# Kernel tuning notes

Hardware: AMD Instinct MI355X
Metric: run time of the kernel (lower is better)

Reference implementation:

```python
import jax, jax.numpy as jnp
import numpy as np

IN_C, HID, LSTM_H, OUT_C = 128, 128, 128, 2
N_NODES, N_EDGES, N_GRAPHS = 100000, 1600000, 256


def gcn_conv(x, src, dst, W, b, n_nodes):
    # h = XW, then symmetric-normalized aggregation with self loops (PyG GCNConv defaults)
    h = x @ W  # [N, H]
    loop = jnp.arange(n_nodes)
    s = jnp.concatenate([src, loop])
    d = jnp.concatenate([dst, loop])
    deg = jax.ops.segment_sum(jnp.ones_like(d, dtype=h.dtype), d, num_segments=n_nodes)
    dinv = jnp.where(deg > 0, jax.lax.rsqrt(deg), 0.0)
    norm = dinv[s] * dinv[d]  # [E+N]
    out = jax.ops.segment_sum(norm[:, None] * h[s], d, num_segments=n_nodes)
    return out + b


def setup_inputs() -> dict:
    key = jax.random.key(0)
    ks = jax.random.split(key, 16)
    x = jax.random.normal(ks[0], (N_NODES, IN_C), dtype=jnp.float32)
    edge_index = jax.random.randint(ks[1], (2, N_EDGES), 0, N_NODES)
    batch = jnp.sort(jax.random.randint(ks[2], (N_NODES,), 0, N_GRAPHS))
    sc = lambda *shape: 1.0 / np.sqrt(shape[0])
    W0 = jax.random.normal(ks[3], (IN_C, HID), jnp.float32) * sc(IN_C)
    b0 = jnp.zeros((HID,), jnp.float32)
    W1 = jax.random.normal(ks[4], (HID, HID), jnp.float32) * sc(HID)
    b1 = jnp.zeros((HID,), jnp.float32)
    W2 = jax.random.normal(ks[5], (HID, HID), jnp.float32) * sc(HID)
    b2 = jnp.zeros((HID,), jnp.float32)
    W_ih = jax.random.normal(ks[6], (4 * LSTM_H, HID), jnp.float32) * sc(HID)
    W_hh = jax.random.normal(ks[7], (4 * LSTM_H, LSTM_H), jnp.float32) * sc(LSTM_H)
    b_ih = jnp.zeros((4 * LSTM_H,), jnp.float32)
    b_hh = jnp.zeros((4 * LSTM_H,), jnp.float32)
    W_fc = jax.random.normal(ks[8], (OUT_C, LSTM_H), jnp.float32) * sc(LSTM_H)
    b_fc = jnp.zeros((OUT_C,), jnp.float32)
    return dict(x=x, edge_index=edge_index, batch=batch, num_graphs=N_GRAPHS,
                W0=W0, b0=b0, W1=W1, b1=b1, W2=W2, b2=b2,
                W_ih=W_ih, W_hh=W_hh, b_ih=b_ih, b_hh=b_hh, W_fc=W_fc, b_fc=b_fc)


def reference(x, edge_index, batch, num_graphs, W0, b0, W1, b1, W2, b2,
              W_ih, W_hh, b_ih, b_hh, W_fc, b_fc):
    n_nodes = x.shape[0]
    src, dst = edge_index[0], edge_index[1]
    h = x
    for W, b in ((W0, b0), (W1, b1), (W2, b2)):
        h = jax.nn.relu(gcn_conv(h, src, dst, W, b, n_nodes))
    # dropout: identity in eval mode
    # global_mean_pool over batch ids
    sums = jax.ops.segment_sum(h, batch, num_segments=num_graphs)  # [G, HID]
    cnts = jax.ops.segment_sum(jnp.ones((n_nodes,), h.dtype), batch, num_segments=num_graphs)
    pooled = sums / jnp.maximum(cnts, 1.0)[:, None]
    # single-step LSTM from zero state: h0 = c0 = 0 => W_hh contributes 0
    g = pooled @ W_ih.T + b_ih + b_hh  # [G, 4H]
    i, f, gg, o = jnp.split(g, 4, axis=-1)  # PyTorch gate order i,f,g,o
    c = jax.nn.sigmoid(i) * jnp.tanh(gg)
    hn = jax.nn.sigmoid(o) * jnp.tanh(c)
    return hn @ W_fc.T + b_fc
```

## Files before the change

kernel.cpp:

```cpp
#include <hip/hip_runtime.h>
#include <math.h>
#include <stdint.h>

#define HID 128
#define SCAN_CHUNK 1024
#define NBUCK_MAX 512
#define EDGE_TILE 8192
#define GEMM_ROWS 128
#define XS_STRIDE 136

typedef short bf16x8 __attribute__((ext_vector_type(8)));
typedef float f32x4 __attribute__((ext_vector_type(4)));

__device__ __forceinline__ unsigned int f2bf(float f) {
    union { float f; uint32_t i; } u; u.f = f;
    uint32_t r = u.i + 0x7fffu + ((u.i >> 16) & 1u);
    return r >> 16;
}

__global__ __launch_bounds__(256) void scan_phase1(const int* __restrict__ cnt,
                                                   int* __restrict__ blockSums,
                                                   float* __restrict__ dinv, int nN) {
    __shared__ int sdata[256];
    const int t = threadIdx.x;
    const int idx = blockIdx.x * SCAN_CHUNK + t * 4;
    int v0 = 0, v1 = 0, v2 = 0, v3 = 0;
    if (idx + 3 < nN) {
        int4 v = *(const int4*)(cnt + idx);
        v0 = v.x; v1 = v.y; v2 = v.z; v3 = v.w;
        float4 dv;
        dv.x = rsqrtf((float)v0 + 1.0f);
        dv.y = rsqrtf((float)v1 + 1.0f);
        dv.z = rsqrtf((float)v2 + 1.0f);
        dv.w = rsqrtf((float)v3 + 1.0f);
        *(float4*)(dinv + idx) = dv;
    } else {
        if (idx     < nN) { v0 = cnt[idx];     dinv[idx]     = rsqrtf((float)v0 + 1.0f); }
        if (idx + 1 < nN) { v1 = cnt[idx + 1]; dinv[idx + 1] = rsqrtf((float)v1 + 1.0f); }
        if (idx + 2 < nN) { v2 = cnt[idx + 2]; dinv[idx + 2] = rsqrtf((float)v2 + 1.0f); }
        if (idx + 3 < nN) { v3 = cnt[idx + 3]; dinv[idx + 3] = rsqrtf((float)v3 + 1.0f); }
    }
    sdata[t] = v0 + v1 + v2 + v3;
    __syncthreads();
#pragma unroll
    for (int off = 128; off > 0; off >>= 1) {
        if (t < off) sdata[t] += sdata[t + off];
        __syncthreads();
    }
    if (t == 0) blockSums[blockIdx.x] = sdata[0];
}

__global__ __launch_bounds__(256) void scan_phase2(int* __restrict__ blockSums, int nB) {
    __shared__ int sd[256];
    const int t = threadIdx.x;
    sd[t] = (t < nB) ? blockSums[t] : 0;
    __syncthreads();
#pragma unroll
    for (int off = 1; off < 256; off <<= 1) {
        int v = sd[t];
        int add = (t >= off) ? sd[t - off] : 0;
        __syncthreads();
        sd[t] = v + add;
        __syncthreads();
    }
    if (t < nB) blockSums[t] = (t > 0) ? sd[t - 1] : 0;
}

__global__ __launch_bounds__(256) void scan_phase3(const int* __restrict__ cnt,
                                                   const int* __restrict__ blockOffsets,
                                                   int* __restrict__ rowptr, int nN, int nE) {
    __shared__ int sdata[256];
    const int t = threadIdx.x;
    const int idx = blockIdx.x * SCAN_CHUNK + t * 4;
    int v0 = 0, v1 = 0, v2 = 0, v3 = 0;
    if (idx + 3 < nN) {
        int4 v = *(const int4*)(cnt + idx);
        v0 = v.x; v1 = v.y; v2 = v.z; v3 = v.w;
    } else {
        if (idx     < nN) v0 = cnt[idx];
        if (idx + 1 < nN) v1 = cnt[idx + 1];
        if (idx + 2 < nN) v2 = cnt[idx + 2];
        if (idx + 3 < nN) v3 = cnt[idx + 3];
    }
    sdata[t] = v0 + v1 + v2 + v3;
    __syncthreads();
#pragma unroll
    for (int off = 1; off < 256; off <<= 1) {
        int v = sdata[t];
        int add = (t >= off) ? sdata[t - off] : 0;
        __syncthreads();
        sdata[t] = v + add;
        __syncthreads();
    }
    const int pre = blockOffsets[blockIdx.x] + ((t > 0) ? sdata[t - 1] : 0);
    if (idx + 3 < nN) {
        *(int4*)(rowptr + idx) = make_int4(pre, pre + v0, pre + v0 + v1, pre + v0 + v1 + v2);
    } else {
        if (idx     < nN) rowptr[idx]     = pre;
        if (idx + 1 < nN) rowptr[idx + 1] = pre + v0;
        if (idx + 2 < nN) rowptr[idx + 2] = pre + v0 + v1;
// ... 110 lines not shown
        int w = i >> 14, r = i & 16383;
        int n = r >> 7, k = r & 127;
        const float* W = (w == 0) ? W0 : (w == 1) ? W1 : W2;
        Wtb[i] = (unsigned short)f2bf(W[k * HID + n]);
    }
}

__global__ __launch_bounds__(256) void gemm_mfma_f32in(const float* __restrict__ X,
                                                       const uint4* __restrict__ Wtb,
                                                       const float* __restrict__ dinv,
                                                       unsigned int* __restrict__ Pb32,
                                                       int nN) {
    __shared__ short Xs[GEMM_ROWS * XS_STRIDE];
    __shared__ short Ws[HID * XS_STRIDE];
    const int tid = threadIdx.x;
    const int rowBase = blockIdx.x * GEMM_ROWS;
#pragma unroll
    for (int it = 0; it < 16; ++it) {
        int f = it * 256 + tid;
        int row = f >> 5, c = f & 31;
        int grow = rowBase + row;
        float4 v = make_float4(0.f, 0.f, 0.f, 0.f);
        if (grow < nN) v = *(const float4*)(X + (size_t)grow * HID + c * 4);
        uint2 o;
        o.x = f2bf(v.x) | (f2bf(v.y) << 16);
        o.y = f2bf(v.z) | (f2bf(v.w) << 16);
        *(uint2*)(&Xs[row * XS_STRIDE + c * 4]) = o;
    }
#pragma unroll
    for (int it = 0; it < 8; ++it) {
        int f = it * 256 + tid;
        int n = f >> 4, c = f & 15;
        *(uint4*)(&Ws[n * XS_STRIDE + c * 8]) = Wtb[f];
    }
    __syncthreads();
    const int wave = tid >> 6, lane = tid & 63;
    const int quad = lane >> 4, l16 = lane & 15;
    f32x4 acc[2][8] = {};
    const int kq = quad * 8;
#pragma unroll
    for (int ks = 0; ks < 4; ++ks) {
        const int k0 = ks * 32 + kq;
        bf16x8 a0 = *(const bf16x8*)(&Xs[(wave * 32 + l16) * XS_STRIDE + k0]);
        bf16x8 a1 = *(const bf16x8*)(&Xs[(wave * 32 + 16 + l16) * XS_STRIDE + k0]);
#pragma unroll
        for (int nt = 0; nt < 8; ++nt) {
            bf16x8 b = *(const bf16x8*)(&Ws[(nt * 16 + l16) * XS_STRIDE + k0]);
            acc[0][nt] = __builtin_amdgcn_mfma_f32_16x16x32_bf16(a0, b, acc[0][nt], 0, 0, 0);
            acc[1][nt] = __builtin_amdgcn_mfma_f32_16x16x32_bf16(a1, b, acc[1][nt], 0, 0, 0);
        }
    }
#pragma unroll
    for (int mt = 0; mt < 2; ++mt) {
        const int gr0 = rowBase + wave * 32 + mt * 16 + quad * 4;
#pragma unroll
        for (int r = 0; r < 4; ++r) {
            const int gr = gr0 + r;
            const bool ok = gr < nN;
            const float d = ok ? dinv[gr] : 0.f;
#pragma unroll
            for (int nt = 0; nt < 8; ++nt) {
                float v = d * acc[mt][nt][r];
                float vo = __shfl_xor(v, 1, 64);
                if (ok && !(l16 & 1)) {
                    Pb32[(size_t)gr * 64 + nt * 8 + (l16 >> 1)] = f2bf(v) | (f2bf(vo) << 16);
                }
            }
        }
    }
}

__device__ __forceinline__ void acc_bf8(const uint4 q, float* a) {
    union { uint32_t i; float f; } t;
    t.i = q.x << 16;          a[0] += t.f;
    t.i = q.x & 0xffff0000u;  a[1] += t.f;
    t.i = q.y << 16;          a[2] += t.f;
    t.i = q.y & 0xffff0000u;  a[3] += t.f;
    t.i = q.z << 16;          a[4] += t.f;
    t.i = q.z & 0xffff0000u;  a[5] += t.f;
    t.i = q.w << 16;          a[6] += t.f;
    t.i = q.w & 0xffff0000u;  a[7] += t.f;
}

__global__ __launch_bounds__(256) void fused_agg_gemm(const uint4* __restrict__ Pb,
                                                      const int* __restrict__ rowptr,
                                                      const int* __restrict__ ssrc,
                                                      const float* __restrict__ dinv,
                                                      const float* __restrict__ bias,
                                                      const uint4* __restrict__ Wtb,
                                                      unsigned int* __restrict__ Pout32,
                                                      int nN) {
    __shared__ short Ws[HID * XS_STRIDE];
    __shared__ short Hs[16 * XS_STRIDE];
    const int tid = threadIdx.x;
#pragma unroll
    for (int it = 0; it < 8; ++it) {
        int f = it * 256 + tid;
        int n = f >> 4, c = f & 15;
        *(uint4*)(&Ws[n * XS_STRIDE + c * 8]) = Wtb[f];
    }
    const int lane16 = tid & 15;
    const int grp = tid >> 4;
    const int v = blockIdx.x * 16 + grp;
    const bool ok = v < nN;
    float a0[8], a1[8], a2[8], a3[8];
#pragma unroll
    for (int i = 0; i < 8; ++i) { a0[i] = 0.f; a1[i] = 0.f; a2[i] = 0.f; a3[i] = 0.f; }
    uint4 q = make_uint4(0u, 0u, 0u, 0u);
    if (ok) {
        acc_bf8(Pb[(size_t)v * 16 + lane16], a0);
        int e = rowptr[v];
        const int e1 = rowptr[v + 1];
        for (; e + 4 <= e1; e += 4) {
            const int u0 = ssrc[e + 0], u1 = ssrc[e + 1], u2 = ssrc[e + 2], u3 = ssrc[e + 3];
            uint4 q0 = Pb[(size_t)u0 * 16 + lane16];
            uint4 q1 = Pb[(size_t)u1 * 16 + lane16];
            uint4 q2 = Pb[(size_t)u2 * 16 + lane16];
            uint4 q3 = Pb[(size_t)u3 * 16 + lane16];
            acc_bf8(q0, a0); acc_bf8(q1, a1); acc_bf8(q2, a2); acc_bf8(q3, a3);
        }
        for (; e < e1; ++e) {
            uint4 qe = Pb[(size_t)ssrc[e] * 16 + lane16];
            acc_bf8(qe, a1);
        }
        const float dv = dinv[v];
        const float4 bb0 = ((const float4*)bias)[lane16 * 2];
        const float4 bb1 = ((const float4*)bias)[lane16 * 2 + 1];
        float4 o0, o1;
        o0.x = fmaxf(fmaf(dv, (a0[0] + a1[0]) + (a2[0] + a3[0]), bb0.x), 0.f);
        o0.y = fmaxf(fmaf(dv, (a0[1] + a1[1]) + (a2[1] + a3[1]), bb0.y), 0.f);
        o0.z = fmaxf(fmaf(dv, (a0[2] + a1[2]) + (a2[2] + a3[2]), bb0.z), 0.f);
        o0.w = fmaxf(fmaf(dv, (a0[3] + a1[3]) + (a2[3] + a3[3]), bb0.w), 0.f);
        o1.x = fmaxf(fmaf(dv, (a0[4] + a1[4]) + (a2[4] + a3[4]), bb1.x), 0.f);
        o1.y = fmaxf(fmaf(dv, (a0[5] + a1[5]) + (a2[5] + a3[5]), bb1.y), 0.f);
        o1.z = fmaxf(fmaf(dv, (a0[6] + a1[6]) + (a2[6] + a3[6]), bb1.z), 0.f);
        o1.w = fmaxf(fmaf(dv, (a0[7] + a1[7]) + (a2[7] + a3[7]), bb1.w), 0.f);
        q.x = f2bf(o0.x) | (f2bf(o0.y) << 16);
        q.y = f2bf(o0.z) | (f2bf(o0.w) << 16);
        q.z = f2bf(o1.x) | (f2bf(o1.y) << 16);
        q.w = f2bf(o1.z) | (f2bf(o1.w) << 16);
    }
    *(uint4*)(&Hs[grp * XS_STRIDE + lane16 * 8]) = q;
    __syncthreads();
    const int wave = tid >> 6, lane = tid & 63;
    const int quad = lane >> 4, l16 = lane & 15;
    f32x4 acc[2] = {};
#pragma unroll
    for (int ks = 0; ks < 4; ++ks) {
        const int k0 = ks * 32 + quad * 8;
        bf16x8 a = *(const bf16x8*)(&Hs[l16 * XS_STRIDE + k0]);
#pragma unroll
        for (int nt = 0; nt < 2; ++nt) {
            bf16x8 b = *(const bf16x8*)(&Ws[((wave * 2 + nt) * 16 + l16) * XS_STRIDE + k0]);
            acc[nt] = __builtin_amdgcn_mfma_f32_16x16x32_bf16(a, b, acc[nt], 0, 0, 0);
        }
    }
#pragma unroll
    for (int r = 0; r < 4; ++r) {
        const int gr = blockIdx.x * 16 + quad * 4 + r;
        const bool okr = gr < nN;
        const float d = okr ? dinv[gr] : 0.f;
#pragma unroll
        for (int nt = 0; nt < 2; ++nt) {
            float val = d * acc[nt][r];
            float vo = __shfl_xor(val, 1, 64);
            if (okr && !(l16 & 1)) {
                Pout32[(size_t)gr * 64 + (wave * 2 + nt) * 8 + (l16 >> 1)] =
                    f2bf(val) | (f2bf(vo) << 16);
            }
        }
    }
}

__global__ __launch_bounds__(256) void agg_kernel(const uint4* __restrict__ Pb,
                                                  const int* __restrict__ rowptr,
                                                  const int* __restrict__ ssrc,
                                                  const float* __restrict__ dinv,
                                                  const float* __restrict__ bias,
                                                  uint4* __restrict__ Xb_out, int nN) {
    const int lane = threadIdx.x & 15;
    const int grp = threadIdx.x >> 4;
    const int v = blockIdx.x * 16 + grp;
    if (v >= nN) return;
    float a0[8], a1[8], a2[8], a3[8];
#pragma unroll
    for (int i = 0; i < 8; ++i) { a0[i] = 0.f; a1[i] = 0.f; a2[i] = 0.f; a3[i] = 0.f; }
    acc_bf8(Pb[(size_t)v * 16 + lane], a0);
    int e = rowptr[v];
    const int e1 = rowptr[v + 1];
    for (; e + 4 <= e1; e += 4) {
        const int u0 = ssrc[e + 0], u1 = ssrc[e + 1], u2 = ssrc[e + 2], u3 = ssrc[e + 3];
        uint4 q0 = Pb[(size_t)u0 * 16 + lane];
        uint4 q1 = Pb[(size_t)u1 * 16 + lane];
        uint4 q2 = Pb[(size_t)u2 * 16 + lane];
        uint4 q3 = Pb[(size_t)u3 * 16 + lane];
        acc_bf8(q0, a0); acc_bf8(q1, a1); acc_bf8(q2, a2); acc_bf8(q3, a3);
    }
    for (; e < e1; ++e) {
        uint4 q = Pb[(size_t)ssrc[e] * 16 + lane];
        acc_bf8(q, a1);
    }
    const float dv = dinv[v];
    const float4 bb0 = ((const float4*)bias)[lane * 2];
    const float4 bb1 = ((const float4*)bias)[lane * 2 + 1];
    float4 o0, o1;
    o0.x = fmaxf(fmaf(dv, (a0[0] + a1[0]) + (a2[0] + a3[0]), bb0.x), 0.f);
    o0.y = fmaxf(fmaf(dv, (a0[1] + a1[1]) + (a2[1] + a3[1]), bb0.y), 0.f);
    o0.z = fmaxf(fmaf(dv, (a0[2] + a1[2]) + (a2[2] + a3[2]), bb0.z), 0.f);
    o0.w = fmaxf(fmaf(dv, (a0[3] + a1[3]) + (a2[3] + a3[3]), bb0.w), 0.f);
    o1.x = fmaxf(fmaf(dv, (a0[4] + a1[4]) + (a2[4] + a3[4]), bb1.x), 0.f);
    o1.y = fmaxf(fmaf(dv, (a0[5] + a1[5]) + (a2[5] + a3[5]), bb1.y), 0.f);
    o1.z = fmaxf(fmaf(dv, (a0[6] + a1[6]) + (a2[6] + a3[6]), bb1.z), 0.f);
    o1.w = fmaxf(fmaf(dv, (a0[7] + a1[7]) + (a2[7] + a3[7]), bb1.w), 0.f);
    uint4 q;
    q.x = f2bf(o0.x) | (f2bf(o0.y) << 16);
    q.y = f2bf(o0.z) | (f2bf(o0.w) << 16);
    q.z = f2bf(o1.x) | (f2bf(o1.y) << 16);
    q.w = f2bf(o1.z) | (f2bf(o1.w) << 16);
    Xb_out[(size_t)v * 16 + lane] = q;
}

__global__ __launch_bounds__(256) void pool_partial(const unsigned int* __restrict__ Xb32,
                                                    const int* __restrict__ batch,
                                                    float* __restrict__ psum, int nN) {
    const int c2 = threadIdx.x & 63;
    int n = blockIdx.x * 64 + (threadIdx.x >> 6);
    const int nEnd = min(blockIdx.x * 64 + 64, nN);
    float acc0 = 0.f, acc1 = 0.f;
    int g = -1;
    for (; n < nEnd; n += 4) {
        int gn = batch[n];
        unsigned int q = Xb32[(size_t)n * 64 + c2];
        union { uint32_t i; float f; } lo, hi;
        lo.i = q << 16; hi.i = q & 0xffff0000u;
        if (gn != g) {
            if (g >= 0) {
                atomicAdd(&psum[g * HID + c2 * 2], acc0);
                atomicAdd(&psum[g * HID + c2 * 2 + 1], acc1);
            }
            g = gn;
            acc0 = lo.f; acc1 = hi.f;
        } else {
            acc0 += lo.f; acc1 += hi.f;
        }
    }
    if (g >= 0) {
        atomicAdd(&psum[g * HID + c2 * 2], acc0);
        atomicAdd(&psum[g * HID + c2 * 2 + 1], acc1);
    }
}

__global__ __launch_bounds__(128) void pool_finalize(const float* __restrict__ psum,
                                                     const int* __restrict__ batch,
                                                     float* __restrict__ pooled, int nN) {
    const int g = blockIdx.x;
    int lo = 0, hi = nN;
    while (lo < hi) { int m = (lo + hi) >> 1; if (batch[m] < g) lo = m + 1; else hi = m; }
    const int start = lo;
    hi = nN;
    while (lo < hi) { int m = (lo + hi) >> 1; if (batch[m] < g + 1) lo = m + 1; else hi = m; }
    const float c = (float)max(lo - start, 1);
    pooled[g * HID + threadIdx.x] = psum[g * HID + threadIdx.x] / c;
}

__device__ __forceinline__ float sigmoidf_(float x) { return 1.0f / (1.0f + expf(-x)); }

__global__ __launch_bounds__(128) void lstm_fc_kernel(const float* __restrict__ pooled,
                                                      const float* __restrict__ W_ih,
                                                      const float* __restrict__ b_ih,
                                                      const float* __restrict__ b_hh,
                                                      const float* __restrict__ W_fc,
                                                      const float* __restrict__ b_fc,
                                                      float* __restrict__ out) {
    __shared__ float pv[HID];
    __shared__ float r0[2], r1[2];
    const int g = blockIdx.x, j = threadIdx.x;
    pv[j] = pooled[g * HID + j];
    __syncthreads();
    float di = b_ih[j] + b_hh[j];
    float dg = b_ih[256 + j] + b_hh[256 + j];
    float dO = b_ih[384 + j] + b_hh[384 + j];
    const float4* pv4 = (const float4*)pv;
#pragma unroll 4
    for (int k4 = 0; k4 < 32; ++k4) {
        float4 p = pv4[k4];
        float4 wi = *(const float4*)(W_ih + (size_t)j * HID + k4 * 4);
        float4 wg = *(const float4*)(W_ih + (size_t)(256 + j) * HID + k4 * 4);
        float4 wo = *(const float4*)(W_ih + (size_t)(384 + j) * HID + k4 * 4);
        di += p.x * wi.x + p.y * wi.y + p.z * wi.z + p.w * wi.w;
        dg += p.x * wg.x + p.y * wg.y + p.z * wg.z + p.w * wg.w;
        dO += p.x * wo.x + p.y * wo.y + p.z * wo.z + p.w * wo.w;
    }
    float c = sigmoidf_(di) * tanhf(dg);
    float hn = sigmoidf_(dO) * tanhf(c);
    float p0 = hn * W_fc[j];
    float p1 = hn * W_fc[HID + j];
#pragma unroll
    for (int off = 32; off > 0; off >>= 1) {
        p0 += __shfl_down(p0, off, 64);
        p1 += __shfl_down(p1, off, 64);
    }
    const int w = j >> 6, l = j & 63;
    if (l == 0) { r0[w] = p0; r1[w] = p1; }
    __syncthreads();
    if (j == 0) {
        out[g * 2 + 0] = r0[0] + r0[1] + b_fc[0];
        out[g * 2 + 1] = r1[0] + r1[1] + b_fc[1];
    }
}

extern "C" void kernel_launch(void* const* d_in, const int* in_sizes, int n_in,
                              void* d_out, int out_size, void* d_ws, size_t ws_size,
                              hipStream_t stream) {
    const float* x      = (const float*)d_in[0];
    const int*   eidx   = (const int*)d_in[1];
    const int*   batch  = (const int*)d_in[2];
    const float* W0     = (const float*)d_in[4];
    const float* b0     = (const float*)d_in[5];
    const float* W1     = (const float*)d_in[6];
    const float* b1     = (const float*)d_in[7];
    const float* W2     = (const float*)d_in[8];
    const float* b2     = (const float*)d_in[9];
    const float* W_ih   = (const float*)d_in[10];
    const float* b_ih   = (const float*)d_in[12];
    const float* b_hh   = (const float*)d_in[13];
    const float* W_fc   = (const float*)d_in[14];
    const float* b_fc   = (const float*)d_in[15];
    float* out = (float*)d_out;

    const int nN = in_sizes[0] / HID;
    const int nE = in_sizes[1] / 2;
    const int nG = out_size / 2;
    const int* src = eidx;
    const int* dst = eidx + nE;
    const int rowsPad = (nN + GEMM_ROWS - 1) & ~(GEMM_ROWS - 1);

    size_t off = 0;
    auto alloc = [&](size_t bytes) -> void* {
        void* p = (char*)d_ws + off;
        off += (bytes + 255) & ~(size_t)255;
        return p;
    };
    uint4* Pb     = (uint4*)alloc((size_t)nN * 16 * sizeof(uint4));
    uint4* Pb2    = (uint4*)alloc((size_t)nN * 16 * sizeof(uint4));
    uint4* Xb     = (uint4*)alloc((size_t)nN * 16 * sizeof(uint4));
    float* dinv   = (float*)alloc((size_t)nN * sizeof(float));
    int*   cnt    = (int*)alloc((size_t)nN * sizeof(int));
    int*   rowptr = (int*)alloc((size_t)(nN + 1) * sizeof(int));
    int*   ssrc   = (int*)alloc((size_t)nE * sizeof(int));
    unsigned int* ebuf = (unsigned int*)alloc((size_t)nE * sizeof(unsigned int));
    float* pooled = (float*)alloc((size_t)nG * HID * sizeof(float));
    float* psum   = (float*)alloc((size_t)nG * HID * sizeof(float));
    int*   blockSums = (int*)alloc(1024 * sizeof(int));
    int*   bcnt   = (int*)alloc(NBUCK_MAX * sizeof(int));
    int*   boff   = (int*)alloc(NBUCK_MAX * sizeof(int));
    int*   bcur   = (int*)alloc(NBUCK_MAX * sizeof(int));
    unsigned short* Wtb = (unsigned short*)alloc(3 * HID * HID * sizeof(unsigned short));
    (void)ws_size;

    const int scanBlocks = (nN + SCAN_CHUNK - 1) / SCAN_CHUNK;
    const int nB = (nN + 255) >> 8;
    const int tileBlocks = (nE + EDGE_TILE - 1) / EDGE_TILE;

    hipMemsetAsync(bcnt, 0, NBUCK_MAX * sizeof(int), stream);
    bucket_count<<<tileBlocks, 256, 0, stream>>>(dst, bcnt, nE, nB);
    bucket_scan<<<1, 512, 0, stream>>>(bcnt, boff, bcur, nB);
    bucket_scatter<<<tileBlocks, 256, 0, stream>>>(src, dst, bcur, ebuf, nE, nB);

    node_count<<<nB, 256, 0, stream>>>(ebuf, boff, cnt, nE, nB, nN);
    scan_phase1<<<scanBlocks, 256, 0, stream>>>(cnt, blockSums, dinv, nN);
    scan_phase2<<<1, 256, 0, stream>>>(blockSums, scanBlocks);
    scan_phase3<<<scanBlocks, 256, 0, stream>>>(cnt, blockSums, rowptr, nN, nE);
    csr_from_buckets<<<nB, 256, 0, stream>>>(ebuf, boff, rowptr, ssrc, nE, nB);

    wt_kernel<<<(3 * HID * HID + 255) / 256, 256, 0, stream>>>(W0, W1, W2, Wtb);

    const int gemmBlocks = rowsPad / GEMM_ROWS;
    const int aggBlocks = (nN + 15) / 16;
    const uint4* Wt1 = (const uint4*)(Wtb + HID * HID);
    const uint4* Wt2 = (const uint4*)(Wtb + 2 * HID * HID);

    gemm_mfma_f32in<<<gemmBlocks, 256, 0, stream>>>(x, (const uint4*)Wtb, dinv,
                                                    (unsigned int*)Pb, nN);
    fused_agg_gemm<<<aggBlocks, 256, 0, stream>>>(Pb, rowptr, ssrc, dinv, b0, Wt1,
                                                  (unsigned int*)Pb2, nN);
    fused_agg_gemm<<<aggBlocks, 256, 0, stream>>>(Pb2, rowptr, ssrc, dinv, b1, Wt2,
                                                  (unsigned int*)Pb, nN);
    agg_kernel<<<aggBlocks, 256, 0, stream>>>(Pb, rowptr, ssrc, dinv, b2, Xb, nN);

    hipMemsetAsync(psum, 0, (size_t)nG * HID * sizeof(float), stream);
    pool_partial<<<(nN + 63) / 64, 256, 0, stream>>>((const unsigned int*)Xb, batch, psum, nN);
    pool_finalize<<<nG, 128, 0, stream>>>(psum, batch, pooled, nN);
    lstm_fc_kernel<<<nG, 128, 0, stream>>>(pooled, W_ih, b_ih, b_hh, W_fc, b_fc, out);
}
```

Baseline: 465.3 us.

## Shuffle-broadcast edge indices, gather 8 rows in flight, load W fragments from global

Each 16-lane group now loads 8 neighbour indices in one coalesced read and broadcasts them with wave shuffles. It then issues 8 independent row gathers per iteration instead of 4 scalar-index gathers, and accumulates into 2 register arrays instead of 4. The fused aggregation+GEMM kernel no longer stages the whole 128x128 weight tile in LDS. Each wave loads its own MFMA B fragments straight from global memory into registers, which sharply cuts LDS per block and should raise occupancy. The cost is redundant global weight reads per block, which rely on L2 caching, plus some extra shuffle instructions.

New measurement: 471.5 us. Within noise of the previous version (+1.3%).

```diff
diff --git a/kernel.cpp b/kernel.cpp
--- a/kernel.cpp
+++ b/kernel.cpp
@@ -292,6 +292,60 @@
     t.i = q.w & 0xffff0000u;  a[7] += t.f;
 }
 
+__device__ __forceinline__ void gather_accum(const uint4* __restrict__ Pb,
+                                             const int* __restrict__ rowptr,
+                                             const int* __restrict__ ssrc,
+                                             int v, int lane16, int gbase,
+                                             float* __restrict__ a0,
+                                             float* __restrict__ a1) {
+    acc_bf8(Pb[(size_t)v * 16 + lane16], a0);
+    int e = rowptr[v];
+    const int e1 = rowptr[v + 1];
+    const int sl = lane16 & 7;
+    for (; e + 8 <= e1; e += 8) {
+        const int s = ssrc[e + sl];
+        const int u0 = __shfl(s, gbase + 0, 64);
+        const int u1 = __shfl(s, gbase + 1, 64);
+        const int u2 = __shfl(s, gbase + 2, 64);
+        const int u3 = __shfl(s, gbase + 3, 64);
+        uint4 q0 = Pb[(size_t)u0 * 16 + lane16];
+        uint4 q1 = Pb[(size_t)u1 * 16 + lane16];
+        uint4 q2 = Pb[(size_t)u2 * 16 + lane16];
+        uint4 q3 = Pb[(size_t)u3 * 16 + lane16];
+        const int u4 = __shfl(s, gbase + 4, 64);
+        const int u5 = __shfl(s, gbase + 5, 64);
+        const int u6 = __shfl(s, gbase + 6, 64);
+        const int u7 = __shfl(s, gbase + 7, 64);
+        uint4 q4 = Pb[(size_t)u4 * 16 + lane16];
+        uint4 q5 = Pb[(size_t)u5 * 16 + lane16];
+        uint4 q6 = Pb[(size_t)u6 * 16 + lane16];
+        uint4 q7 = Pb[(size_t)u7 * 16 + lane16];
+        acc_bf8(q0, a0); acc_bf8(q1, a1); acc_bf8(q2, a0); acc_bf8(q3, a1);
+        acc_bf8(q4, a0); acc_bf8(q5, a1); acc_bf8(q6, a0); acc_bf8(q7, a1);
+    }
+    const int rem = e1 - e;
+    if (rem > 0) {
+        const int s = ssrc[(sl < rem) ? (e + sl) : e];
+        int j = 0;
+        if (rem >= 4) {
+            const int u0 = __shfl(s, gbase + 0, 64);
+            const int u1 = __shfl(s, gbase + 1, 64);
+            const int u2 = __shfl(s, gbase + 2, 64);
+            const int u3 = __shfl(s, gbase + 3, 64);
+            uint4 q0 = Pb[(size_t)u0 * 16 + lane16];
+            uint4 q1 = Pb[(size_t)u1 * 16 + lane16];
+            uint4 q2 = Pb[(size_t)u2 * 16 + lane16];
+            uint4 q3 = Pb[(size_t)u3 * 16 + lane16];
+            acc_bf8(q0, a0); acc_bf8(q1, a1); acc_bf8(q2, a0); acc_bf8(q3, a1);
+            j = 4;
+        }
+        for (; j < rem; ++j) {
+            const int u = __shfl(s, gbase + j, 64);
+            acc_bf8(Pb[(size_t)u * 16 + lane16], a1);
+        }
+    }
+}
+
 __global__ __launch_bounds__(256) void fused_agg_gemm(const uint4* __restrict__ Pb,
                                                       const int* __restrict__ rowptr,
                                                       const int* __restrict__ ssrc,
@@ -300,51 +354,31 @@
                                                       const uint4* __restrict__ Wtb,
                                                       unsigned int* __restrict__ Pout32,
                                                       int nN) {
-    __shared__ short Ws[HID * XS_STRIDE];
     __shared__ short Hs[16 * XS_STRIDE];
     const int tid = threadIdx.x;
-#pragma unroll
-    for (int it = 0; it < 8; ++it) {
-        int f = it * 256 + tid;
-        int n = f >> 4, c = f & 15;
-        *(uint4*)(&Ws[n * XS_STRIDE + c * 8]) = Wtb[f];
-    }
     const int lane16 = tid & 15;
     const int grp = tid >> 4;
+    const int gbase = tid & 48;
     const int v = blockIdx.x * 16 + grp;
     const bool ok = v < nN;
-    float a0[8], a1[8], a2[8], a3[8];
-#pragma unroll
-    for (int i = 0; i < 8; ++i) { a0[i] = 0.f; a1[i] = 0.f; a2[i] = 0.f; a3[i] = 0.f; }
+    float a0[8], a1[8];
+#pragma unroll
+    for (int i = 0; i < 8; ++i) { a0[i] = 0.f; a1[i] = 0.f; }
+    if (ok) gather_accum(Pb, rowptr, ssrc, v, lane16, gbase, a0, a1);
     uint4 q = make_uint4(0u, 0u, 0u, 0u);
     if (ok) {
-        acc_bf8(Pb[(size_t)v * 16 + lane16], a0);
-        int e = rowptr[v];
-        const int e1 = rowptr[v + 1];
-        for (; e + 4 <= e1; e += 4) {
-            const int u0 = ssrc[e + 0], u1 = ssrc[e + 1], u2 = ssrc[e + 2], u3 = ssrc[e + 3];
-            uint4 q0 = Pb[(size_t)u0 * 16 + lane16];
-            uint4 q1 = Pb[(size_t)u1 * 16 + lane16];
-            uint4 q2 = Pb[(size_t)u2 * 16 + lane16];
-            uint4 q3 = Pb[(size_t)u3 * 16 + lane16];
-            acc_bf8(q0, a0); acc_bf8(q1, a1); acc_bf8(q2, a2); acc_bf8(q3, a3);
-        }
-        for (; e < e1; ++e) {
-            uint4 qe = Pb[(size_t)ssrc[e] * 16 + lane16];
-            acc_bf8(qe, a1);
-        }
         const float dv = dinv[v];
         const float4 bb0 = ((const float4*)bias)[lane16 * 2];
         const float4 bb1 = ((const float4*)bias)[lane16 * 2 + 1];
         float4 o0, o1;
-        o0.x = fmaxf(fmaf(dv, (a0[0] + a1[0]) + (a2[0] + a3[0]), bb0.x), 0.f);
-        o0.y = fmaxf(fmaf(dv, (a0[1] + a1[1]) + (a2[1] + a3[1]), bb0.y), 0.f);
-        o0.z = fmaxf(fmaf(dv, (a0[2] + a1[2]) + (a2[2] + a3[2]), bb0.z), 0.f);
-        o0.w = fmaxf(fmaf(dv, (a0[3] + a1[3]) + (a2[3] + a3[3]), bb0.w), 0.f);
-        o1.x = fmaxf(fmaf(dv, (a0[4] + a1[4]) + (a2[4] + a3[4]), bb1.x), 0.f);
-        o1.y = fmaxf(fmaf(dv, (a0[5] + a1[5]) + (a2[5] + a3[5]), bb1.y), 0.f);
-        o1.z = fmaxf(fmaf(dv, (a0[6] + a1[6]) + (a2[6] + a3[6]), bb1.z), 0.f);
-        o1.w = fmaxf(fmaf(dv, (a0[7] + a1[7]) + (a2[7] + a3[7]), bb1.w), 0.f);
+        o0.x = fmaxf(fmaf(dv, a0[0] + a1[0], bb0.x), 0.f);
+        o0.y = fmaxf(fmaf(dv, a0[1] + a1[1], bb0.y), 0.f);
+        o0.z = fmaxf(fmaf(dv, a0[2] + a1[2], bb0.z), 0.f);
+        o0.w = fmaxf(fmaf(dv, a0[3] + a1[3], bb0.w), 0.f);
+        o1.x = fmaxf(fmaf(dv, a0[4] + a1[4], bb1.x), 0.f);
+        o1.y = fmaxf(fmaf(dv, a0[5] + a1[5], bb1.y), 0.f);
+        o1.z = fmaxf(fmaf(dv, a0[6] + a1[6], bb1.z), 0.f);
+        o1.w = fmaxf(fmaf(dv, a0[7] + a1[7], bb1.w), 0.f);
         q.x = f2bf(o0.x) | (f2bf(o0.y) << 16);
         q.y = f2bf(o0.z) | (f2bf(o0.w) << 16);
         q.z = f2bf(o1.x) | (f2bf(o1.y) << 16);
@@ -354,16 +388,22 @@
     __syncthreads();
     const int wave = tid >> 6, lane = tid & 63;
     const int quad = lane >> 4, l16 = lane & 15;
+    bf16x8 bfr[2][4];
+#pragma unroll
+    for (int nt = 0; nt < 2; ++nt) {
+#pragma unroll
+        for (int ks = 0; ks < 4; ++ks) {
+            uint4 t = Wtb[((wave * 2 + nt) * 16 + l16) * 16 + ks * 4 + quad];
+            bfr[nt][ks] = *(bf16x8*)&t;
+        }
+    }
     f32x4 acc[2] = {};
 #pragma unroll
     for (int ks = 0; ks < 4; ++ks) {
         const int k0 = ks * 32 + quad * 8;
         bf16x8 a = *(const bf16x8*)(&Hs[l16 * XS_STRIDE + k0]);
-#pragma unroll
-        for (int nt = 0; nt < 2; ++nt) {
-            bf16x8 b = *(const bf16x8*)(&Ws[((wave * 2 + nt) * 16 + l16) * XS_STRIDE + k0]);
-            acc[nt] = __builtin_amdgcn_mfma_f32_16x16x32_bf16(a, b, acc[nt], 0, 0, 0);
-        }
+        acc[0] = __builtin_amdgcn_mfma_f32_16x16x32_bf16(a, bfr[0][ks], acc[0], 0, 0, 0);
+        acc[1] = __builtin_amdgcn_mfma_f32_16x16x32_bf16(a, bfr[1][ks], acc[1], 0, 0, 0);
     }
 #pragma unroll
     for (int r = 0; r < 4; ++r) {
@@ -388,46 +428,33 @@
                                                   const float* __restrict__ dinv,
                                                   const float* __restrict__ bias,
                                                   uint4* __restrict__ Xb_out, int nN) {
-    const int lane = threadIdx.x & 15;
+    const int lane16 = threadIdx.x & 15;
     const int grp = threadIdx.x >> 4;
+    const int gbase = threadIdx.x & 48;
     const int v = blockIdx.x * 16 + grp;
     if (v >= nN) return;
-    float a0[8], a1[8], a2[8], a3[8];
-#pragma unroll
-    for (int i = 0; i < 8; ++i) { a0[i] = 0.f; a1[i] = 0.f; a2[i] = 0.f; a3[i] = 0.f; }
-    acc_bf8(Pb[(size_t)v * 16 + lane], a0);
-    int e = rowptr[v];
-    const int e1 = rowptr[v + 1];
-    for (; e + 4 <= e1; e += 4) {
-        const int u0 = ssrc[e + 0], u1 = ssrc[e + 1], u2 = ssrc[e + 2], u3 = ssrc[e + 3];
-        uint4 q0 = Pb[(size_t)u0 * 16 + lane];
-        uint4 q1 = Pb[(size_t)u1 * 16 + lane];
-        uint4 q2 = Pb[(size_t)u2 * 16 + lane];
-        uint4 q3 = Pb[(size_t)u3 * 16 + lane];
-        acc_bf8(q0, a0); acc_bf8(q1, a1); acc_bf8(q2, a2); acc_bf8(q3, a3);
-    }
-    for (; e < e1; ++e) {
-        uint4 q = Pb[(size_t)ssrc[e] * 16 + lane];
-        acc_bf8(q, a1);
-    }
+    float a0[8], a1[8];
+#pragma unroll
+    for (int i = 0; i < 8; ++i) { a0[i] = 0.f; a1[i] = 0.f; }
+    gather_accum(Pb, rowptr, ssrc, v, lane16, gbase, a0, a1);
     const float dv = dinv[v];
-    const float4 bb0 = ((const float4*)bias)[lane * 2];
-    const float4 bb1 = ((const float4*)bias)[lane * 2 + 1];
+    const float4 bb0 = ((const float4*)bias)[lane16 * 2];
+    const float4 bb1 = ((const float4*)bias)[lane16 * 2 + 1];
     float4 o0, o1;
-    o0.x = fmaxf(fmaf(dv, (a0[0] + a1[0]) + (a2[0] + a3[0]), bb0.x), 0.f);
-    o0.y = fmaxf(fmaf(dv, (a0[1] + a1[1]) + (a2[1] + a3[1]), bb0.y), 0.f);
-    o0.z = fmaxf(fmaf(dv, (a0[2] + a1[2]) + (a2[2] + a3[2]), bb0.z), 0.f);
-    o0.w = fmaxf(fmaf(dv, (a0[3] + a1[3]) + (a2[3] + a3[3]), bb0.w), 0.f);
-    o1.x = fmaxf(fmaf(dv, (a0[4] + a1[4]) + (a2[4] + a3[4]), bb1.x), 0.f);
-    o1.y = fmaxf(fmaf(dv, (a0[5] + a1[5]) + (a2[5] + a3[5]), bb1.y), 0.f);
-    o1.z = fmaxf(fmaf(dv, (a0[6] + a1[6]) + (a2[6] + a3[6]), bb1.z), 0.f);
-    o1.w = fmaxf(fmaf(dv, (a0[7] + a1[7]) + (a2[7] + a3[7]), bb1.w), 0.f);
+    o0.x = fmaxf(fmaf(dv, a0[0] + a1[0], bb0.x), 0.f);
+    o0.y = fmaxf(fmaf(dv, a0[1] + a1[1], bb0.y), 0.f);
+    o0.z = fmaxf(fmaf(dv, a0[2] + a1[2], bb0.z), 0.f);
+    o0.w = fmaxf(fmaf(dv, a0[3] + a1[3], bb0.w), 0.f);
+    o1.x = fmaxf(fmaf(dv, a0[4] + a1[4], bb1.x), 0.f);
+    o1.y = fmaxf(fmaf(dv, a0[5] + a1[5], bb1.y), 0.f);
+    o1.z = fmaxf(fmaf(dv, a0[6] + a1[6], bb1.z), 0.f);
+    o1.w = fmaxf(fmaf(dv, a0[7] + a1[7], bb1.w), 0.f);
     uint4 q;
     q.x = f2bf(o0.x) | (f2bf(o0.y) << 16);
     q.y = f2bf(o0.z) | (f2bf(o0.w) << 16);
     q.z = f2bf(o1.x) | (f2bf(o1.y) << 16);
     q.w = f2bf(o1.z) | (f2bf(o1.w) << 16);
-    Xb_out[(size_t)v * 16 + lane] = q;
+    Xb_out[(size_t)v * 16 + lane16] = q;
 }
 
 __global__ __launch_bounds__(256) void pool_partial(const unsigned int* __restrict__ Xb32,
```

## Fuse mean pooling, LSTM and FC into one per-graph kernel

Applied to the files above, without the earlier changes.

Replaces the memset, atomic partial pooling, finalize and LSTM/FC kernels with a single kernel that runs one block per graph. Each block binary-searches its node range in the sorted batch array, sums the rows with four strided row groups, reduces them in shared memory, and applies the LSTM gate and FC math directly. This removes three launches, a memset and the global atomics. In exchange it uses only 256 blocks, so reading the roughly 25 MB node-feature buffer gets much less parallelism than the old approach.

Result: no change. 457.0 us (-1.8%).

```diff
diff --git a/kernel.cpp b/kernel.cpp
--- a/kernel.cpp
+++ b/kernel.cpp
@@ -16,6 +16,12 @@
     union { float f; uint32_t i; } u; u.f = f;
     uint32_t r = u.i + 0x7fffu + ((u.i >> 16) & 1u);
     return r >> 16;
+}
+__device__ __forceinline__ float bf2f_lo(uint32_t x) {
+    union { uint32_t i; float f; } t; t.i = x << 16; return t.f;
+}
+__device__ __forceinline__ float bf2f_hi(uint32_t x) {
+    union { uint32_t i; float f; } t; t.i = x & 0xffff0000u; return t.f;
 }
 
 __global__ __launch_bounds__(256) void scan_phase1(const int* __restrict__ cnt,
@@ -430,92 +436,93 @@
     Xb_out[(size_t)v * 16 + lane] = q;
 }
 
-__global__ __launch_bounds__(256) void pool_partial(const unsigned int* __restrict__ Xb32,
-                                                    const int* __restrict__ batch,
-                                                    float* __restrict__ psum, int nN) {
-    const int c2 = threadIdx.x & 63;
-    int n = blockIdx.x * 64 + (threadIdx.x >> 6);
-    const int nEnd = min(blockIdx.x * 64 + 64, nN);
+__global__ __launch_bounds__(256) void pool_lstm(const unsigned int* __restrict__ Xb32,
+                                                 const int* __restrict__ batch,
+                                                 const float* __restrict__ W_ih,
+                                                 const float* __restrict__ b_ih,
+                                                 const float* __restrict__ b_hh,
+                                                 const float* __restrict__ W_fc,
+                                                 const float* __restrict__ b_fc,
+                                                 float* __restrict__ out, int nN) {
+    __shared__ float sred[4][HID];
+    __shared__ float pv[HID];
+    __shared__ float r0[4], r1[4];
+    __shared__ int sbounds[2];
+    const int g = blockIdx.x;
+    const int tid = threadIdx.x;
+    if (tid == 0) {
+        int lo = 0, hi = nN;
+        while (lo < hi) { int m = (lo + hi) >> 1; if (batch[m] < g) lo = m + 1; else hi = m; }
+        sbounds[0] = lo;
+        hi = nN;
+        while (lo < hi) { int m = (lo + hi) >> 1; if (batch[m] < g + 1) lo = m + 1; else hi = m; }
+        sbounds[1] = lo;
+    }
+    __syncthreads();
+    const int s = sbounds[0], e = sbounds[1];
+    const int c2 = tid & 63;
+    const int st = tid >> 6;
     float acc0 = 0.f, acc1 = 0.f;
-    int g = -1;
-    for (; n < nEnd; n += 4) {
-        int gn = batch[n];
-        unsigned int q = Xb32[(size_t)n * 64 + c2];
-        union { uint32_t i; float f; } lo, hi;
-        lo.i = q << 16; hi.i = q & 0xffff0000u;
-        if (gn != g) {
-            if (g >= 0) {
-                atomicAdd(&psum[g * HID + c2 * 2], acc0);
-                atomicAdd(&psum[g * HID + c2 * 2 + 1], acc1);
-            }
-            g = gn;
-            acc0 = lo.f; acc1 = hi.f;
-        } else {
-            acc0 += lo.f; acc1 += hi.f;
+    int v = s + st;
+    for (; v + 12 < e; v += 16) {
+        unsigned int q0 = Xb32[(size_t)(v     ) * 64 + c2];
+        unsigned int q1 = Xb32[(size_t)(v +  4) * 64 + c2];
+        unsigned int q2 = Xb32[(size_t)(v +  8) * 64 + c2];
+        unsigned int q3 = Xb32[(size_t)(v + 12) * 64 + c2];
+        acc0 += (bf2f_lo(q0) + bf2f_lo(q1)) + (bf2f_lo(q2) + bf2f_lo(q3));
+        acc1 += (bf2f_hi(q0) + bf2f_hi(q1)) + (bf2f_hi(q2) + bf2f_hi(q3));
+    }
+    for (; v < e; v += 4) {
+        unsigned int q = Xb32[(size_t)v * 64 + c2];
+        acc0 += bf2f_lo(q);
+        acc1 += bf2f_hi(q);
+    }
+    sred[st][c2 * 2] = acc0;
+    sred[st][c2 * 2 + 1] = acc1;
+    __syncthreads();
+    if (st == 0) {
+        const float inv = 1.0f / (float)max(e - s, 1);
+        pv[c2 * 2]     = ((sred[0][c2 * 2] + sred[1][c2 * 2]) +
+                          (sred[2][c2 * 2] + sred[3][c2 * 2])) * inv;
+        pv[c2 * 2 + 1] = ((sred[0][c2 * 2 + 1] + sred[1][c2 * 2 + 1]) +
+                          (sred[2][c2 * 2 + 1] + sred[3][c2 * 2 + 1])) * inv;
+    }
+    __syncthreads();
+    float p0 = 0.f, p1 = 0.f;
+    if (tid < HID) {
+        const int j = tid;
+        float di = b_ih[j] + b_hh[j];
+        float dg = b_ih[256 + j] + b_hh[256 + j];
+        float dO = b_ih[384 + j] + b_hh[384 + j];
+        const float4* pv4 = (const float4*)pv;
+#pragma unroll 4
+        for (int k4 = 0; k4 < 32; ++k4) {
+            float4 p = pv4[k4];
+            float4 wi = *(const float4*)(W_ih + (size_t)j * HID + k4 * 4);
+            float4 wg = *(const float4*)(W_ih + (size_t)(256 + j) * HID + k4 * 4);
+            float4 wo = *(const float4*)(W_ih + (size_t)(384 + j) * HID + k4 * 4);
+            di += p.x * wi.x + p.y * wi.y + p.z * wi.z + p.w * wi.w;
+            dg += p.x * wg.x + p.y * wg.y + p.z * wg.z + p.w * wg.w;
+            dO += p.x * wo.x + p.y * wo.y + p.z * wo.z + p.w * wo.w;
         }
-    }
-    if (g >= 0) {
-        atomicAdd(&psum[g * HID + c2 * 2], acc0);
-        atomicAdd(&psum[g * HID + c2 * 2 + 1], acc1);
-    }
-}
-
-__global__ __launch_bounds__(128) void pool_finalize(const float* __restrict__ psum,
-                                                     const int* __restrict__ batch,
-                                                     float* __restrict__ pooled, int nN) {
-    const int g = blockIdx.x;
-    int lo = 0, hi = nN;
-    while (lo < hi) { int m = (lo + hi) >> 1; if (batch[m] < g) lo = m + 1; else hi = m; }
-    const int start = lo;
-    hi = nN;
-    while (lo < hi) { int m = (lo + hi) >> 1; if (batch[m] < g + 1) lo = m + 1; else hi = m; }
-    const float c = (float)max(lo - start, 1);
-    pooled[g * HID + threadIdx.x] = psum[g * HID + threadIdx.x] / c;
-}
-
-__device__ __forceinline__ float sigmoidf_(float x) { return 1.0f / (1.0f + expf(-x)); }
-
-__global__ __launch_bounds__(128) void lstm_fc_kernel(const float* __restrict__ pooled,
-                                                      const float* __restrict__ W_ih,
-                                                      const float* __restrict__ b_ih,
-                                                      const float* __restrict__ b_hh,
-                                                      const float* __restrict__ W_fc,
-                                                      const float* __restrict__ b_fc,
-                                                      float* __restrict__ out) {
-    __shared__ float pv[HID];
-    __shared__ float r0[2], r1[2];
-    const int g = blockIdx.x, j = threadIdx.x;
-    pv[j] = pooled[g * HID + j];
-    __syncthreads();
-    float di = b_ih[j] + b_hh[j];
-    float dg = b_ih[256 + j] + b_hh[256 + j];
-    float dO = b_ih[384 + j] + b_hh[384 + j];
-    const float4* pv4 = (const float4*)pv;
-#pragma unroll 4
-    for (int k4 = 0; k4 < 32; ++k4) {
-        float4 p = pv4[k4];
-        float4 wi = *(const float4*)(W_ih + (size_t)j * HID + k4 * 4);
-        float4 wg = *(const float4*)(W_ih + (size_t)(256 + j) * HID + k4 * 4);
-        float4 wo = *(const float4*)(W_ih + (size_t)(384 + j) * HID + k4 * 4);
-        di += p.x * wi.x + p.y * wi.y + p.z * wi.z + p.w * wi.w;
-        dg += p.x * wg.x + p.y * wg.y + p.z * wg.z + p.w * wg.w;
-        dO += p.x * wo.x + p.y * wo.y + p.z * wo.z + p.w * wo.w;
-    }
-    float c = sigmoidf_(di) * tanhf(dg);
-    float hn = sigmoidf_(dO) * tanhf(c);
-    float p0 = hn * W_fc[j];
-    float p1 = hn * W_fc[HID + j];
+        const float si = 1.0f / (1.0f + expf(-di));
+        const float so = 1.0f / (1.0f + expf(-dO));
+        const float c = si * tanhf(dg);
+        const float hn = so * tanhf(c);
+        p0 = hn * W_fc[j];
+        p1 = hn * W_fc[HID + j];
+    }
 #pragma unroll
     for (int off = 32; off > 0; off >>= 1) {
         p0 += __shfl_down(p0, off, 64);
         p1 += __shfl_down(p1, off, 64);
     }
-    const int w = j >> 6, l = j & 63;
+    const int w = tid >> 6, l = tid & 63;
     if (l == 0) { r0[w] = p0; r1[w] = p1; }
     __syncthreads();
-    if (j == 0) {
-        out[g * 2 + 0] = r0[0] + r0[1] + b_fc[0];
-        out[g * 2 + 1] = r1[0] + r1[1] + b_fc[1];
+    if (tid == 0) {
+        out[g * 2 + 0] = (r0[0] + r0[1]) + (r0[2] + r0[3]) + b_fc[0];
+        out[g * 2 + 1] = (r1[0] + r1[1]) + (r1[2] + r1[3]) + b_fc[1];
     }
 }
 
@@ -559,8 +566,6 @@
     int*   rowptr = (int*)alloc((size_t)(nN + 1) * sizeof(int));
     int*   ssrc   = (int*)alloc((size_t)nE * sizeof(int));
     unsigned int* ebuf = (unsigned int*)alloc((size_t)nE * sizeof(unsigned int));
-    float* pooled = (float*)alloc((size_t)nG * HID * sizeof(float));
-    float* psum   = (float*)alloc((size_t)nG * HID * sizeof(float));
     int*   blockSums = (int*)alloc(1024 * sizeof(int));
     int*   bcnt   = (int*)alloc(NBUCK_MAX * sizeof(int));
     int*   boff   = (int*)alloc(NBUCK_MAX * sizeof(int));
@@ -598,8 +603,6 @@
                                                   (unsigned int*)Pb, nN);
     agg_kernel<<<aggBlocks, 256, 0, stream>>>(Pb, rowptr, ssrc, dinv, b2, Xb, nN);
 
-    hipMemsetAsync(psum, 0, (size_t)nG * HID * sizeof(float), stream);
-    pool_partial<<<(nN + 63) / 64, 256, 0, stream>>>((const unsigned int*)Xb, batch, psum, nN);
-    pool_finalize<<<nG, 128, 0, stream>>>(psum, batch, pooled, nN);
-    lstm_fc_kernel<<<nG, 128, 0, stream>>>(pooled, W_ih, b_ih, b_hh, W_fc, b_fc, out);
-}
+    pool_lstm<<<nG, 256, 0, stream>>>((const unsigned int*)Xb, batch,
+                                      W_ih, b_ih, b_hh, W_fc, b_fc, out, nN);
+}
```

## Fuse final aggregation with mean-pool and merge pool finalize into LSTM kernel

Applied to the files above, without the earlier changes.

The last GCN aggregation now reduces each block's 16 node outputs in shared memory by graph id and atomically adds them into the per-graph sums. This removes the bf16 Xb write and re-read and the separate pool_partial kernel. The count division is moved into the LSTM kernel, dropping pool_finalize and the pooled buffer, and the psum memset is hoisted to the start. Pooling now sums fp32 values rather than bf16-rounded ones, and the block issues more atomics because each block covers only 16 nodes.

Result: faster. 453.2 us (-2.6%).

```diff
diff --git a/kernel.cpp b/kernel.cpp
--- a/kernel.cpp
+++ b/kernel.cpp
@@ -16,6 +16,12 @@
     union { float f; uint32_t i; } u; u.f = f;
     uint32_t r = u.i + 0x7fffu + ((u.i >> 16) & 1u);
     return r >> 16;
+}
+__device__ __forceinline__ float bf2f_lo(uint32_t x) {
+    union { uint32_t i; float f; } t; t.i = x << 16; return t.f;
+}
+__device__ __forceinline__ float bf2f_hi(uint32_t x) {
+    union { uint32_t i; float f; } t; t.i = x & 0xffff0000u; return t.f;
 }
 
 __global__ __launch_bounds__(256) void scan_phase1(const int* __restrict__ cnt,
@@ -382,110 +388,97 @@
     }
 }
 
-__global__ __launch_bounds__(256) void agg_kernel(const uint4* __restrict__ Pb,
-                                                  const int* __restrict__ rowptr,
-                                                  const int* __restrict__ ssrc,
-                                                  const float* __restrict__ dinv,
-                                                  const float* __restrict__ bias,
-                                                  uint4* __restrict__ Xb_out, int nN) {
-    const int lane = threadIdx.x & 15;
+__global__ __launch_bounds__(256) void agg_pool(const uint4* __restrict__ Pb,
+                                                const int* __restrict__ rowptr,
+                                                const int* __restrict__ ssrc,
+                                                const float* __restrict__ dinv,
+                                                const float* __restrict__ bias,
+                                                const int* __restrict__ batch,
+                                                float* __restrict__ psum, int nN) {
+    __shared__ float hsf[16][HID];
+    __shared__ int sg[16];
+    const int lane16 = threadIdx.x & 15;
     const int grp = threadIdx.x >> 4;
     const int v = blockIdx.x * 16 + grp;
-    if (v >= nN) return;
+    const bool ok = v < nN;
     float a0[8], a1[8], a2[8], a3[8];
 #pragma unroll
     for (int i = 0; i < 8; ++i) { a0[i] = 0.f; a1[i] = 0.f; a2[i] = 0.f; a3[i] = 0.f; }
-    acc_bf8(Pb[(size_t)v * 16 + lane], a0);
-    int e = rowptr[v];
-    const int e1 = rowptr[v + 1];
-    for (; e + 4 <= e1; e += 4) {
-        const int u0 = ssrc[e + 0], u1 = ssrc[e + 1], u2 = ssrc[e + 2], u3 = ssrc[e + 3];
-        uint4 q0 = Pb[(size_t)u0 * 16 + lane];
-        uint4 q1 = Pb[(size_t)u1 * 16 + lane];
-        uint4 q2 = Pb[(size_t)u2 * 16 + lane];
-        uint4 q3 = Pb[(size_t)u3 * 16 + lane];
-        acc_bf8(q0, a0); acc_bf8(q1, a1); acc_bf8(q2, a2); acc_bf8(q3, a3);
-    }
-    for (; e < e1; ++e) {
-        uint4 q = Pb[(size_t)ssrc[e] * 16 + lane];
-        acc_bf8(q, a1);
-    }
-    const float dv = dinv[v];
-    const float4 bb0 = ((const float4*)bias)[lane * 2];
-    const float4 bb1 = ((const float4*)bias)[lane * 2 + 1];
-    float4 o0, o1;
-    o0.x = fmaxf(fmaf(dv, (a0[0] + a1[0]) + (a2[0] + a3[0]), bb0.x), 0.f);
-    o0.y = fmaxf(fmaf(dv, (a0[1] + a1[1]) + (a2[1] + a3[1]), bb0.y), 0.f);
-    o0.z = fmaxf(fmaf(dv, (a0[2] + a1[2]) + (a2[2] + a3[2]), bb0.z), 0.f);
-    o0.w = fmaxf(fmaf(dv, (a0[3] + a1[3]) + (a2[3] + a3[3]), bb0.w), 0.f);
-    o1.x = fmaxf(fmaf(dv, (a0[4] + a1[4]) + (a2[4] + a3[4]), bb1.x), 0.f);
-    o1.y = fmaxf(fmaf(dv, (a0[5] + a1[5]) + (a2[5] + a3[5]), bb1.y), 0.f);
-    o1.z = fmaxf(fmaf(dv, (a0[6] + a1[6]) + (a2[6] + a3[6]), bb1.z), 0.f);
-    o1.w = fmaxf(fmaf(dv, (a0[7] + a1[7]) + (a2[7] + a3[7]), bb1.w), 0.f);
-    uint4 q;
-    q.x = f2bf(o0.x) | (f2bf(o0.y) << 16);
-    q.y = f2bf(o0.z) | (f2bf(o0.w) << 16);
-    q.z = f2bf(o1.x) | (f2bf(o1.y) << 16);
-    q.w = f2bf(o1.z) | (f2bf(o1.w) << 16);
-    Xb_out[(size_t)v * 16 + lane] = q;
-}
-
-__global__ __launch_bounds__(256) void pool_partial(const unsigned int* __restrict__ Xb32,
-                                                    const int* __restrict__ batch,
-                                                    float* __restrict__ psum, int nN) {
-    const int c2 = threadIdx.x & 63;
-    int n = blockIdx.x * 64 + (threadIdx.x >> 6);
-    const int nEnd = min(blockIdx.x * 64 + 64, nN);
-    float acc0 = 0.f, acc1 = 0.f;
-    int g = -1;
-    for (; n < nEnd; n += 4) {
-        int gn = batch[n];
-        unsigned int q = Xb32[(size_t)n * 64 + c2];
-        union { uint32_t i; float f; } lo, hi;
-        lo.i = q << 16; hi.i = q & 0xffff0000u;
-        if (gn != g) {
-            if (g >= 0) {
-                atomicAdd(&psum[g * HID + c2 * 2], acc0);
-                atomicAdd(&psum[g * HID + c2 * 2 + 1], acc1);
+    float hv[8];
+#pragma unroll
+    for (int i = 0; i < 8; ++i) hv[i] = 0.f;
+    if (ok) {
+        acc_bf8(Pb[(size_t)v * 16 + lane16], a0);
+        int e = rowptr[v];
+        const int e1 = rowptr[v + 1];
+        for (; e + 4 <= e1; e += 4) {
+            const int u0 = ssrc[e + 0], u1 = ssrc[e + 1], u2 = ssrc[e + 2], u3 = ssrc[e + 3];
+            uint4 q0 = Pb[(size_t)u0 * 16 + lane16];
+            uint4 q1 = Pb[(size_t)u1 * 16 + lane16];
+            uint4 q2 = Pb[(size_t)u2 * 16 + lane16];
+            uint4 q3 = Pb[(size_t)u3 * 16 + lane16];
+            acc_bf8(q0, a0); acc_bf8(q1, a1); acc_bf8(q2, a2); acc_bf8(q3, a3);
+        }
+        for (; e < e1; ++e) {
+            uint4 q = Pb[(size_t)ssrc[e] * 16 + lane16];
+            acc_bf8(q, a1);
+        }
+        const float dv = dinv[v];
+        const float4 bb0 = ((const float4*)bias)[lane16 * 2];
+        const float4 bb1 = ((const float4*)bias)[lane16 * 2 + 1];
+        hv[0] = fmaxf(fmaf(dv, (a0[0] + a1[0]) + (a2[0] + a3[0]), bb0.x), 0.f);
+        hv[1] = fmaxf(fmaf(dv, (a0[1] + a1[1]) + (a2[1] + a3[1]), bb0.y), 0.f);
+        hv[2] = fmaxf(fmaf(dv, (a0[2] + a1[2]) + (a2[2] + a3[2]), bb0.z), 0.f);
+        hv[3] = fmaxf(fmaf(dv, (a0[3] + a1[3]) + (a2[3] + a3[3]), bb0.w), 0.f);
+        hv[4] = fmaxf(fmaf(dv, (a0[4] + a1[4]) + (a2[4] + a3[4]), bb1.x), 0.f);
+        hv[5] = fmaxf(fmaf(dv, (a0[5] + a1[5]) + (a2[5] + a3[5]), bb1.y), 0.f);
+        hv[6] = fmaxf(fmaf(dv, (a0[6] + a1[6]) + (a2[6] + a3[6]), bb1.z), 0.f);
+        hv[7] = fmaxf(fmaf(dv, (a0[7] + a1[7]) + (a2[7] + a3[7]), bb1.w), 0.f);
+    }
+#pragma unroll
+    for (int j = 0; j < 8; ++j) hsf[grp][lane16 * 8 + j] = hv[j];
+    if (lane16 == 0) sg[grp] = ok ? batch[v] : -1;
+    __syncthreads();
+    if (threadIdx.x < HID) {
+        const int c = threadIdx.x;
+        float acc = 0.f;
+        int g = sg[0];
+#pragma unroll
+        for (int i = 0; i < 16; ++i) {
+            const int gi = sg[i];
+            if (gi != g) {
+                if (g >= 0) atomicAdd(&psum[(size_t)g * HID + c], acc);
+                g = gi;
+                acc = 0.f;
             }
-            g = gn;
-            acc0 = lo.f; acc1 = hi.f;
-        } else {
-            acc0 += lo.f; acc1 += hi.f;
-        }
-    }
-    if (g >= 0) {
-        atomicAdd(&psum[g * HID + c2 * 2], acc0);
-        atomicAdd(&psum[g * HID + c2 * 2 + 1], acc1);
-    }
-}
-
-__global__ __launch_bounds__(128) void pool_finalize(const float* __restrict__ psum,
-                                                     const int* __restrict__ batch,
-                                                     float* __restrict__ pooled, int nN) {
-    const int g = blockIdx.x;
-    int lo = 0, hi = nN;
-    while (lo < hi) { int m = (lo + hi) >> 1; if (batch[m] < g) lo = m + 1; else hi = m; }
-    const int start = lo;
-    hi = nN;
-    while (lo < hi) { int m = (lo + hi) >> 1; if (batch[m] < g + 1) lo = m + 1; else hi = m; }
-    const float c = (float)max(lo - start, 1);
-    pooled[g * HID + threadIdx.x] = psum[g * HID + threadIdx.x] / c;
-}
-
-__device__ __forceinline__ float sigmoidf_(float x) { return 1.0f / (1.0f + expf(-x)); }
-
-__global__ __launch_bounds__(128) void lstm_fc_kernel(const float* __restrict__ pooled,
-                                                      const float* __restrict__ W_ih,
-                                                      const float* __restrict__ b_ih,
-                                                      const float* __restrict__ b_hh,
-                                                      const float* __restrict__ W_fc,
-                                                      const float* __restrict__ b_fc,
-                                                      float* __restrict__ out) {
+            acc += hsf[i][c];
+        }
+        if (g >= 0) atomicAdd(&psum[(size_t)g * HID + c], acc);
+    }
+}
+
+__global__ __launch_bounds__(128) void pool_lstm(const float* __restrict__ psum,
+                                                 const int* __restrict__ batch,
+                                                 const float* __restrict__ W_ih,
+                                                 const float* __restrict__ b_ih,
+                                                 const float* __restrict__ b_hh,
+                                                 const float* __restrict__ W_fc,
+                                                 const float* __restrict__ b_fc,
+                                                 float* __restrict__ out, int nN) {
     __shared__ float pv[HID];
     __shared__ float r0[2], r1[2];
+    __shared__ int scnt;
     const int g = blockIdx.x, j = threadIdx.x;
-    pv[j] = pooled[g * HID + j];
+    if (j == 0) {
+        int lo = 0, hi = nN;
+        while (lo < hi) { int m = (lo + hi) >> 1; if (batch[m] < g) lo = m + 1; else hi = m; }
+        const int start = lo;
+        hi = nN;
+        while (lo < hi) { int m = (lo + hi) >> 1; if (batch[m] < g + 1) lo = m + 1; else hi = m; }
+        scnt = max(lo - start, 1);
+    }
+    __syncthreads();
+    pv[j] = psum[(size_t)g * HID + j] / (float)scnt;
     __syncthreads();
     float di = b_ih[j] + b_hh[j];
     float dg = b_ih[256 + j] + b_hh[256 + j];
@@ -501,8 +494,10 @@
         dg += p.x * wg.x + p.y * wg.y + p.z * wg.z + p.w * wg.w;
         dO += p.x * wo.x + p.y * wo.y + p.z * wo.z + p.w * wo.w;
     }
-    float c = sigmoidf_(di) * tanhf(dg);
-    float hn = sigmoidf_(dO) * tanhf(c);
+    const float si = 1.0f / (1.0f + expf(-di));
+    const float so = 1.0f / (1.0f + expf(-dO));
+    const float c = si * tanhf(dg);
+    const float hn = so * tanhf(c);
     float p0 = hn * W_fc[j];
     float p1 = hn * W_fc[HID + j];
 #pragma unroll
@@ -553,13 +548,11 @@
     };
     uint4* Pb     = (uint4*)alloc((size_t)nN * 16 * sizeof(uint4));
     uint4* Pb2    = (uint4*)alloc((size_t)nN * 16 * sizeof(uint4));
-    uint4* Xb     = (uint4*)alloc((size_t)nN * 16 * sizeof(uint4));
     float* dinv   = (float*)alloc((size_t)nN * sizeof(float));
     int*   cnt    = (int*)alloc((size_t)nN * sizeof(int));
     int*   rowptr = (int*)alloc((size_t)(nN + 1) * sizeof(int));
     int*   ssrc   = (int*)alloc((size_t)nE * sizeof(int));
     unsigned int* ebuf = (unsigned int*)alloc((size_t)nE * sizeof(unsigned int));
-    float* pooled = (float*)alloc((size_t)nG * HID * sizeof(float));
     float* psum   = (float*)alloc((size_t)nG * HID * sizeof(float));
     int*   blockSums = (int*)alloc(1024 * sizeof(int));
     int*   bcnt   = (int*)alloc(NBUCK_MAX * sizeof(int));
@@ -573,6 +566,7 @@
     const int tileBlocks = (nE + EDGE_TILE - 1) / EDGE_TILE;
 
     hipMemsetAsync(bcnt, 0, NBUCK_MAX * sizeof(int), stream);
+    hipMemsetAsync(psum, 0, (size_t)nG * HID * sizeof(float), stream);
     bucket_count<<<tileBlocks, 256, 0, stream>>>(dst, bcnt, nE, nB);
     bucket_scan<<<1, 512, 0, stream>>>(bcnt, boff, bcur, nB);
     bucket_scatter<<<tileBlocks, 256, 0, stream>>>(src, dst, bcur, ebuf, nE, nB);
@@ -596,10 +590,8 @@
                                                   (unsigned int*)Pb2, nN);
     fused_agg_gemm<<<aggBlocks, 256, 0, stream>>>(Pb2, rowptr, ssrc, dinv, b1, Wt2,
                                                   (unsigned int*)Pb, nN);
-    agg_kernel<<<aggBlocks, 256, 0, stream>>>(Pb, rowptr, ssrc, dinv, b2, Xb, nN);
-
-    hipMemsetAsync(psum, 0, (size_t)nG * HID * sizeof(float), stream);
-    pool_partial<<<(nN + 63) / 64, 256, 0, stream>>>((const unsigned int*)Xb, batch, psum, nN);
-    pool_finalize<<<nG, 128, 0, stream>>>(psum, batch, pooled, nN);
-    lstm_fc_kernel<<<nG, 128, 0, stream>>>(pooled, W_ih, b_ih, b_hh, W_fc, b_fc, out);
-}
+    agg_pool<<<aggBlocks, 256, 0, stream>>>(Pb, rowptr, ssrc, dinv, b2, batch, psum, nN);
+
+    pool_lstm<<<nG, 128, 0, stream>>>(psum, batch, W_ih, b_ih, b_hh, W_fc, b_fc,
+                                      out, nN);
+}
```
